# Optimization experiments

Hardware: AMD Instinct MI355X
Metric: run time of the kernel (lower is better)

## Reference

```python
import jax, jax.numpy as jnp
import numpy as np

FEATURE_SIZE = 128  # H = W = feature_size per __init__
BATCH = 8


def setup_inputs() -> dict:
    key = jax.random.key(0)
    # uniform [0,1): threshold >0.5 marks ~half the pixels as 'boundary'
    feature_map = jax.random.uniform(key, (BATCH, 1, FEATURE_SIZE, FEATURE_SIZE), dtype=jnp.float32)
    return {"feature_map": feature_map}


def reference(feature_map):
    """Distance transform: for each pixel (i,j), min Euclidean distance to any
    boundary pixel (feature_map > 0.5), where the boundary set is pooled over
    batch+channel (matching torch.where on the full tensor) and the resulting
    scalar is broadcast to every batch element (matching output[:, :, i, j] = min).
    """
    B, C, H, W = feature_map.shape
    ch = jnp.arange(H, dtype=feature_map.dtype)
    cw = jnp.arange(W, dtype=feature_map.dtype)
    dx2 = (ch[:, None] - ch[None, :]) ** 2  # [H(h), H(i)]
    dy2 = (cw[:, None] - cw[None, :]) ** 2  # [W(w), W(j)]
    # boundary positions, unioned over batch/channel (grid is batch-independent)
    mask = jnp.any(feature_map > 0.5, axis=(0, 1))  # [H, W]
    # all-pairs squared distances: axes (h, w, i, j)
    d2 = dx2[:, None, :, None] + dy2[None, :, None, :]  # [H, W, H, W]
    masked = jnp.where(mask[:, :, None, None], d2, jnp.inf)
    dist = jnp.sqrt(jnp.min(masked, axis=(0, 1)))  # [H, W]; sqrt(min)=min(sqrt)
    return jnp.broadcast_to(dist[None, None], (B, C, H, W))
```

## Files before the change

kernel.cpp:

```cpp
#include <hip/hip_runtime.h>
#include <math.h>

#define H_DIM 128
#define W_DIM 128
#define BATCH 8
#define NPIX (H_DIM * W_DIM)
#define INF_I (1 << 28)

__global__ __launch_bounds__(256) void dist_transform_kernel(
    const float* __restrict__ fm, float* __restrict__ out) {
    const int i = blockIdx.x;
    const int tid = threadIdx.x;

    __shared__ unsigned char maskS[NPIX];
    __shared__ int gS[W_DIM];
    __shared__ float distS[W_DIM];

    const float4* fm4 = (const float4*)fm;
    #pragma unroll 2
    for (int q = 0; q < 16; ++q) {
        const int idx4 = q * 256 + tid;
        bool m0 = false, m1 = false, m2 = false, m3 = false;
        #pragma unroll
        for (int b = 0; b < BATCH; ++b) {
            float4 v = fm4[b * 4096 + idx4];
            m0 |= v.x > 0.5f;
            m1 |= v.y > 0.5f;
            m2 |= v.z > 0.5f;
            m3 |= v.w > 0.5f;
        }
        uchar4 mm;
        mm.x = (unsigned char)m0;
        mm.y = (unsigned char)m1;
        mm.z = (unsigned char)m2;
        mm.w = (unsigned char)m3;
        ((uchar4*)maskS)[idx4] = mm;
    }
    __syncthreads();

    if (tid < W_DIM) {
        const int w = tid;
        int g = INF_I;
        for (int h = 0; h < H_DIM; ++h) {
            const int d = i - h;
            const int dd = d * d;
            if (maskS[h * W_DIM + w]) g = min(g, dd);
        }
        gS[w] = g;
    }
    __syncthreads();

    if (tid < W_DIM) {
        const int j = tid;
        int best = INF_I;
        for (int w = 0; w < W_DIM; ++w) {
            const int d = j - w;
            best = min(best, gS[w] + d * d);
        }
        distS[j] = (best >= INF_I) ? INFINITY : sqrtf((float)best);
    }
    __syncthreads();

    const int j = tid & 127;
    const int bh = tid >> 7;
    const float v = distS[j];
    #pragma unroll
    for (int k = 0; k < 4; ++k) {
        const int b = bh * 4 + k;
        out[b * NPIX + i * W_DIM + j] = v;
    }
}

extern "C" void kernel_launch(void* const* d_in, const int* in_sizes, int n_in,
                              void* d_out, int out_size, void* d_ws, size_t ws_size,
                              hipStream_t stream) {
    const float* fm = (const float*)d_in[0];
    float* out = (float*)d_out;
    dist_transform_kernel<<<H_DIM, 256, 0, stream>>>(fm, out);
}
```

Before: 64.02 us.

## Split mask reduction into separate kernel and use all threads in distance passes

Adds a small pre-pass kernel that computes the batch-unioned boundary mask once into workspace, instead of every one of the 128 blocks rereading all 8 batches of the input. The main kernel now loads the compact byte mask into shared memory and splits both the column and row minimum passes across both halves of the block, merging partial minima through shared memory. This removes 128-fold redundant global reads and idle threads, at the cost of an extra kernel launch and additional barriers.

```diff
diff --git a/kernel.cpp b/kernel.cpp
--- a/kernel.cpp
+++ b/kernel.cpp
@@ -7,57 +7,78 @@
 #define NPIX (H_DIM * W_DIM)
 #define INF_I (1 << 28)
 
-__global__ __launch_bounds__(256) void dist_transform_kernel(
-    const float* __restrict__ fm, float* __restrict__ out) {
+__global__ __launch_bounds__(256) void mask_kernel(const float* __restrict__ fm,
+                                                   unsigned char* __restrict__ mask) {
+    const int idx4 = blockIdx.x * 256 + threadIdx.x;
+    const float4* fm4 = (const float4*)fm;
+    bool m0 = false, m1 = false, m2 = false, m3 = false;
+    #pragma unroll
+    for (int b = 0; b < BATCH; ++b) {
+        float4 v = fm4[b * 4096 + idx4];
+        m0 |= v.x > 0.5f;
+        m1 |= v.y > 0.5f;
+        m2 |= v.z > 0.5f;
+        m3 |= v.w > 0.5f;
+    }
+    uchar4 mm;
+    mm.x = (unsigned char)m0;
+    mm.y = (unsigned char)m1;
+    mm.z = (unsigned char)m2;
+    mm.w = (unsigned char)m3;
+    ((uchar4*)mask)[idx4] = mm;
+}
+
+__global__ __launch_bounds__(256) void dt_kernel(const unsigned char* __restrict__ mask,
+                                                 float* __restrict__ out) {
     const int i = blockIdx.x;
     const int tid = threadIdx.x;
 
     __shared__ unsigned char maskS[NPIX];
+    __shared__ int gpart[2][W_DIM];
     __shared__ int gS[W_DIM];
+    __shared__ int bpart[2][W_DIM];
     __shared__ float distS[W_DIM];
 
-    const float4* fm4 = (const float4*)fm;
-    #pragma unroll 2
-    for (int q = 0; q < 16; ++q) {
-        const int idx4 = q * 256 + tid;
-        bool m0 = false, m1 = false, m2 = false, m3 = false;
-        #pragma unroll
-        for (int b = 0; b < BATCH; ++b) {
-            float4 v = fm4[b * 4096 + idx4];
-            m0 |= v.x > 0.5f;
-            m1 |= v.y > 0.5f;
-            m2 |= v.z > 0.5f;
-            m3 |= v.w > 0.5f;
+    const float4* m4 = (const float4*)mask;
+    #pragma unroll
+    for (int q = 0; q < 4; ++q)
+        ((float4*)maskS)[q * 256 + tid] = m4[q * 256 + tid];
+    __syncthreads();
+
+    const int w = tid & 127;
+    const int half = tid >> 7;
+
+    {
+        int g = INF_I;
+        const int h0 = half * 64;
+        #pragma unroll 4
+        for (int hh = 0; hh < 64; ++hh) {
+            const int h = h0 + hh;
+            const int d = i - h;
+            if (maskS[h * W_DIM + w]) g = min(g, d * d);
         }
-        uchar4 mm;
-        mm.x = (unsigned char)m0;
-        mm.y = (unsigned char)m1;
-        mm.z = (unsigned char)m2;
-        mm.w = (unsigned char)m3;
-        ((uchar4*)maskS)[idx4] = mm;
+        gpart[half][w] = g;
     }
     __syncthreads();
+    if (tid < W_DIM) gS[tid] = min(gpart[0][tid], gpart[1][tid]);
+    __syncthreads();
 
-    if (tid < W_DIM) {
-        const int w = tid;
-        int g = INF_I;
-        for (int h = 0; h < H_DIM; ++h) {
-            const int d = i - h;
-            const int dd = d * d;
-            if (maskS[h * W_DIM + w]) g = min(g, dd);
+    {
+        const int j = w;
+        int best = INF_I;
+        const int w0 = half * 64;
+        #pragma unroll 4
+        for (int ww = 0; ww < 64; ++ww) {
+            const int wc = w0 + ww;
+            const int d = j - wc;
+            best = min(best, gS[wc] + d * d);
         }
-        gS[w] = g;
+        bpart[half][j] = best;
     }
     __syncthreads();
-
     if (tid < W_DIM) {
-        const int j = tid;
-        int best = INF_I;
-        for (int w = 0; w < W_DIM; ++w) {
-            const int d = j - w;
-            best = min(best, gS[w] + d * d);
-        }
-        distS[j] = (best >= INF_I) ? INFINITY : sqrtf((float)best);
+        const int best = min(bpart[0][tid], bpart[1][tid]);
+        distS[tid] = (best >= INF_I) ? INFINITY : sqrtf((float)best);
     }
     __syncthreads();
 
@@ -76,5 +97,8 @@
                               hipStream_t stream) {
     const float* fm = (const float*)d_in[0];
     float* out = (float*)d_out;
-    dist_transform_kernel<<<H_DIM, 256, 0, stream>>>(fm, out);
+    unsigned char* mask = (unsigned char*)d_ws;
+
+    mask_kernel<<<16, 256, 0, stream>>>(fm, mask);
+    dt_kernel<<<H_DIM, 256, 0, stream>>>(mask, out);
 }
```

Measured after the change: 57.94 us. -9.5%, faster.
